# Kernel optimization log

Measured on AMD Instinct MI355X. Metric: run time of the kernel, lower is better.

Reference implementation:

```python
import jax, jax.numpy as jnp
import numpy as np

D_MODEL = 768
N_HEADS = 8
HEAD_DIM = D_MODEL // N_HEADS
LN_EPS = 1e-5

def setup_inputs() -> dict:
    key = jax.random.key(0)
    k1, k2, k3 = jax.random.split(key, 3)
    B, L = 8, 4096
    x = jax.random.normal(k1, (B, L, D_MODEL), dtype=jnp.float32)
    gamma = jnp.ones((D_MODEL,), dtype=jnp.float32)
    beta = jnp.zeros((D_MODEL,), dtype=jnp.float32)
    # torch Linear weights transposed so forward is x @ W
    w_qkv = jax.random.normal(k2, (D_MODEL, 3 * D_MODEL), dtype=jnp.float32) * (1.0 / np.sqrt(D_MODEL))
    w_out = jax.random.normal(k3, (D_MODEL, D_MODEL), dtype=jnp.float32) * (1.0 / np.sqrt(D_MODEL))
    return {"x": x, "gamma": gamma, "beta": beta, "w_qkv": w_qkv, "w_out": w_out}

def reference(x, gamma, beta, w_qkv, w_out):
    B, L, D = x.shape
    residual = x
    # LayerNorm
    mu = jnp.mean(x, axis=-1, keepdims=True)
    var = jnp.mean(jnp.square(x - mu), axis=-1, keepdims=True)
    xn = (x - mu) * jax.lax.rsqrt(var + LN_EPS) * gamma + beta
    # qkv projection, split, reshape to [B, H, L, d]
    qkv = xn @ w_qkv  # [B, L, 3D]
    q, k, v = jnp.split(qkv, 3, axis=-1)
    def to_heads(t):
        return t.reshape(B, L, N_HEADS, HEAD_DIM).transpose(0, 2, 1, 3)
    q, k, v = to_heads(q), to_heads(k), to_heads(v)
    # feature maps: elu + 1
    q = jax.nn.elu(q) + 1.0
    k = jax.nn.elu(k) + 1.0
    # linear attention: kv aggregation then query readout
    kv = jnp.einsum('bhld,bhlv->bhdv', k, v)          # [B,H,d,d]
    out = jnp.einsum('bhld,bhdv->bhlv', q, kv)         # [B,H,L,d]
    k_sum = jnp.sum(k, axis=2)                         # [B,H,d]
    normalizer = jnp.einsum('bhld,bhd->bhl', q, k_sum) # [B,H,L]
    normalizer = jnp.maximum(normalizer, 1e-6)
    out = out / normalizer[..., None]
    out = out.transpose(0, 2, 1, 3).reshape(B, L, D)
    out = out @ w_out
    return out + residual
```

## Files before the change

### kernel.cpp

```cpp
#include <hip/hip_runtime.h>
#include <stdint.h>

#define D_MODEL 768
#define N3      2304
#define NHEAD   8
#define DH      96
#define BATCH   8
#define SEQ     4096
#define ROWS    (BATCH*SEQ)
#define LN_EPS  1e-5f

typedef __attribute__((ext_vector_type(8))) __bf16 bf16x8;
typedef __attribute__((ext_vector_type(4))) float f32x4;
typedef __attribute__((ext_vector_type(8))) unsigned short ushort8;
typedef __attribute__((ext_vector_type(4))) unsigned short ushort4v;

__device__ __forceinline__ unsigned short f2bf(float f) {
  union { float f; unsigned int u; } v; v.f = f;
  unsigned int r = v.u + 0x7FFFu + ((v.u >> 16) & 1u);
  return (unsigned short)(r >> 16);
}
__device__ __forceinline__ float bf2f(unsigned short u) {
  union { unsigned int u; float f; } v; v.u = ((unsigned int)u) << 16;
  return v.f;
}

#define GLOBAL_LDS16(src, dst) \
  __builtin_amdgcn_global_load_lds((const __attribute__((address_space(1))) void*)(src), \
                                   (__attribute__((address_space(3))) void*)(dst), 16, 0, 0)

#define GATE(n) do { asm volatile("s_waitcnt vmcnt(" #n ")" ::: "memory"); \
                     __builtin_amdgcn_s_barrier(); asm volatile("" ::: "memory"); } while (0)

__global__ __launch_bounds__(256) void prep_kernel(
    const float* __restrict__ wqkv, const float* __restrict__ wout,
    unsigned short* __restrict__ wqkvT, unsigned short* __restrict__ woutT,
    const float* __restrict__ x, const float* __restrict__ gamma,
    const float* __restrict__ beta, unsigned short* __restrict__ xn) {
  if (blockIdx.x < 2304) {
    __shared__ float tile[32][33];
    int v = blockIdx.x;
    int bx = v % 96, by = v / 96;
    const float* in; unsigned short* out; int C, c0;
    if (bx < 72) { in = wqkv; out = wqkvT; C = N3;      c0 = bx * 32; }
    else         { in = wout; out = woutT; C = D_MODEL; c0 = (bx - 72) * 32; }
    int r0 = by * 32;
    int tx = threadIdx.x & 31, ty = threadIdx.x >> 5;
    #pragma unroll
    for (int i = ty; i < 32; i += 8)
      tile[i][tx] = in[(size_t)(r0 + i) * C + c0 + tx];
    __syncthreads();
    #pragma unroll
    for (int i = ty; i < 32; i += 8)
      out[(size_t)(c0 + i) * D_MODEL + r0 + tx] = f2bf(tile[tx][i]);
    return;
  }
  int wave = threadIdx.x >> 6, lane = threadIdx.x & 63;
  int row = (blockIdx.x - 2304) * 4 + wave;
  const float* xr = x + (size_t)row * D_MODEL;
  f32x4 v[3];
  float s = 0.f, sq = 0.f;
  #pragma unroll
  for (int i = 0; i < 3; ++i) {
    v[i] = *(const f32x4*)(xr + (i * 64 + lane) * 4);
    #pragma unroll
    for (int c = 0; c < 4; ++c) { s += v[i][c]; sq += v[i][c] * v[i][c]; }
  }
  #pragma unroll
  for (int o = 32; o; o >>= 1) {
    s  += __shfl_xor(s, o, 64);
    sq += __shfl_xor(sq, o, 64);
  }
  float mu  = s * (1.f / 768.f);
  float var = sq * (1.f / 768.f) - mu * mu;
  float rs  = rsqrtf(var + LN_EPS);
  #pragma unroll
  for (int i = 0; i < 3; ++i) {
    int col = (i * 64 + lane) * 4;
    ushort4v o;
    #pragma unroll
    for (int c = 0; c < 4; ++c)
      o[c] = f2bf((v[i][c] - mu) * rs * gamma[col + c] + beta[col + c]);
    *(ushort4v*)(xn + (size_t)row * D_MODEL + col) = o;
  }
}

__global__ __launch_bounds__(256, 2) void gemm_qkv_w_kernel(
    const unsigned short* __restrict__ A, const unsigned short* __restrict__ Bt,
    unsigned short* __restrict__ qb, unsigned short* __restrict__ kT,
    unsigned short* __restrict__ vT) {
  __shared__ unsigned short As[3 * 4096];
  __shared__ unsigned short Bs[3 * 8192];
  const int K = D_MODEL, nbn = 9;
  int nwg = gridDim.x, id = blockIdx.x;
  int q8 = nwg >> 3;
  int wg = (id & 7) * q8 + (id >> 3);
  int bm = wg / nbn, bn = wg % nbn;

  const int lane = threadIdx.x & 63, wid = threadIdx.x >> 6;
  const int wn = wid;
  const int l15 = lane & 15, hi = lane >> 4;
  const int colS = (hi ^ ((l15 >> 1) & 3)) << 3;
  const int srow = lane >> 2;
  const int scol = ((lane & 3) ^ ((lane >> 3) & 3)) << 3;

  const unsigned short* a0 = A  + (size_t)(bm * 128 +      wid * 16 + srow) * K + scol;
  const unsigned short* a1 = A  + (size_t)(bm * 128 + 64 + wid * 16 + srow) * K + scol;
  const unsigned short* b0 = Bt + (size_t)(bn * 256 + wid * 64 +      srow) * K + scol;
  const unsigned short* b1 = Bt + (size_t)(bn * 256 + wid * 64 + 16 + srow) * K + scol;
  const unsigned short* b2 = Bt + (size_t)(bn * 256 + wid * 64 + 32 + srow) * K + scol;
  const unsigned short* b3 = Bt + (size_t)(bn * 256 + wid * 64 + 48 + srow) * K + scol;
  auto stage = [&](int buf, int kt) {
    GLOBAL_LDS16(a0 + kt * 32, &As[buf * 4096 +        wid * 512]);
    GLOBAL_LDS16(a1 + kt * 32, &As[buf * 4096 + 2048 + wid * 512]);
    GLOBAL_LDS16(b0 + kt * 32, &Bs[buf * 8192 + wid * 2048]);
    GLOBAL_LDS16(b1 + kt * 32, &Bs[buf * 8192 + wid * 2048 + 512]);
    GLOBAL_LDS16(b2 + kt * 32, &Bs[buf * 8192 + wid * 2048 + 1024]);
    GLOBAL_LDS16(b3 + kt * 32, &Bs[buf * 8192 + wid * 2048 + 1536]);
  };

  f32x4 acc[8][4];
  #pragma unroll
  for (int i = 0; i < 8; ++i)
    #pragma unroll
    for (int j = 0; j < 4; ++j) acc[i][j] = (f32x4){0.f, 0.f, 0.f, 0.f};

#define QTILE(BUF, STG) do { \
    bf16x8 af[8], bv[4]; \
    _Pragma("unroll") for (int mf = 0; mf < 8; ++mf) \
      af[mf] = *(const bf16x8*)&As[(BUF) * 4096 + (mf * 16 + l15) * 32 + colS]; \
    _Pragma("unroll") for (int nf = 0; nf < 4; ++nf) \
      bv[nf] = *(const bf16x8*)&Bs[(BUF) * 8192 + (wn * 64 + nf * 16 + l15) * 32 + colS]; \
    STG; \
    __builtin_amdgcn_s_setprio(1); \
    _Pragma("unroll") for (int mf = 0; mf < 8; ++mf) \
      _Pragma("unroll") for (int nf = 0; nf < 4; ++nf) \
        acc[mf][nf] = __builtin_amdgcn_mfma_f32_16x16x32_bf16( \
            af[mf], bv[nf], acc[mf][nf], 0, 0, 0); \
    __builtin_amdgcn_s_setprio(0); \
  } while (0)

  stage(0, 0); stage(1, 1);
  for (int it = 0; it < 7; ++it) {
    int T = 3 * it;
    GATE(6); QTILE(0, stage(2, T + 2));
    GATE(6); QTILE(1, stage(0, T + 3));
    GATE(6); QTILE(2, stage(1, T + 4));
  }
  GATE(6); QTILE(0, stage(2, 23));
  GATE(6); QTILE(1, {});
  GATE(0); QTILE(2, {});
#undef QTILE

  int r0 = bm * 128, c0 = bn * 256 + wn * 64;
  if (bn < 3) {
    #pragma unroll
    for (int mf = 0; mf < 8; ++mf)
      #pragma unroll
      for (int nf = 0; nf < 4; ++nf) {
        int col = c0 + nf * 16 + l15;
        #pragma unroll
        for (int r = 0; r < 4; ++r) {
          int row = r0 + mf * 16 + hi * 4 + r;
          float v = acc[mf][nf][r];
          v = (v > 0.f) ? v + 1.f : __expf(v);
          qb[(size_t)row * D_MODEL + col] = f2bf(v);
        }
      }
  } else {
    const bool isK = (bn < 6);
    unsigned short* T = isK ? kT : vT;
    int cbase = c0 - (isK ? 768 : 1536);
    #pragma unroll
    for (int mf = 0; mf < 8; ++mf) {
      int ll = mf * 16 + hi * 4;
      #pragma unroll
      for (int nf = 0; nf < 4; ++nf) {
        int cc = cbase + nf * 16 + l15;
        int h = cc / 96, d = cc - h * 96;
        ushort4v pk;
        #pragma unroll
        for (int r = 0; r < 4; ++r) {
          float v = acc[mf][nf][r];
          if (isK) v = (v > 0.f) ? v + 1.f : __expf(v);
          pk[r] = f2bf(v);
        }
        *(ushort4v*)&T[(((size_t)bm * 8 + h) * 96 + d) * 128 + ll] = pk;
      }
    }
  }
}

__global__ __launch_bounds__(256) void kvagg3_kernel(
    const unsigned short* __restrict__ kT, const unsigned short* __restrict__ vT,
    float* __restrict__ kvp) {
  __shared__ unsigned short KTs[3 * 6144];
  __shared__ unsigned short VTs[3 * 6144];
  __shared__ unsigned short PH[2048];
  int bh = blockIdx.x >> 3, chunk = blockIdx.x & 7;
  int tid = threadIdx.x;
  int lane = tid & 63, wid = tid >> 6;
  int l15 = lane & 15, hi = lane >> 4;

  {
    int r = tid >> 3, sl = tid & 7;
    unsigned short val = (r == 0) ? (unsigned short)0x3F80 : (unsigned short)0;
    ushort8 v8 = {val, val, val, val, val, val, val, val};
    *(ushort8*)&PH[(r * 8 + sl) * 8] = v8;
  }
  __syncthreads();

  const int b = bh >> 3, h = bh & 7;
  auto stage = [&](int buf, int t) {
    #pragma unroll
    for (int i = 0; i < 3; ++i) {
      int sidx = i * 256 + tid;
      int row = sidx >> 3;
      int L = (sidx & 7) ^ (row & 7);
      size_t g = ((((size_t)b * 32 + chunk * 4 + (t >> 1)) * 8 + h) * 96 + row) * 128
               + (t & 1) * 64 + L * 8;
      GLOBAL_LDS16(kT + g, &KTs[buf * 6144 + (i * 256 + wid * 64) * 8]);
      GLOBAL_LDS16(vT + g, &VTs[buf * 6144 + (i * 256 + wid * 64) * 8]);
    }
  };

  f32x4 acc[6][2];
  #pragma unroll
  for (int i = 0; i < 6; ++i)
    #pragma unroll
    for (int j = 0; j < 2; ++j) acc[i][j] = (f32x4){0.f, 0.f, 0.f, 0.f};

#define KVTILE(BUF) do { \
    _Pragma("unroll") for (int kq = 0; kq < 2; ++kq) { \
      bf16x8 af[6], bv[2]; \
      _Pragma("unroll") for (int mf = 0; mf < 6; ++mf) { \
        int row = mf * 16 + l15; \
        af[mf] = *(const bf16x8*)&KTs[(BUF) * 6144 + row * 64 + ((kq * 4 + hi) ^ (row & 7)) * 8]; } \
      if (wid < 3) { \
        _Pragma("unroll") for (int nf = 0; nf < 2; ++nf) { \
          int row = wid * 32 + nf * 16 + l15; \
          bv[nf] = *(const bf16x8*)&VTs[(BUF) * 6144 + row * 64 + ((kq * 4 + hi) ^ (row & 7)) * 8]; } \
      } else { \
        _Pragma("unroll") for (int nf = 0; nf < 2; ++nf) { \
          int row = nf * 16 + l15; \
          bv[nf] = *(const bf16x8*)&PH[row * 64 + ((kq * 4 + hi) ^ ((row + 96) & 7)) * 8]; } \
      } \
      __builtin_amdgcn_s_setprio(1); \
      _Pragma("unroll") for (int mf = 0; mf < 6; ++mf) \
        _Pragma("unroll") for (int nf = 0; nf < 2; ++nf) \
          acc[mf][nf] = __builtin_amdgcn_mfma_f32_16x16x32_bf16( \
              af[mf], bv[nf], acc[mf][nf], 0, 0, 0); \
      __builtin_amdgcn_s_setprio(0); \
    } } while (0)

  stage(0, 0); stage(1, 1);
  for (int t = 0; t < 6; ++t) {
    stage((t + 2) % 3, t + 2);
    GATE(12);
    KVTILE(t % 3);
  }
  GATE(6); KVTILE(0);
  GATE(0); KVTILE(1);
#undef KVTILE

  float* outp = kvp + ((size_t)bh * 8 + chunk) * (96 * 112);
  #pragma unroll
  for (int nf = 0; nf < 2; ++nf) {
    int e = wid * 32 + nf * 16 + l15;
    if (e < 112) {
      #pragma unroll
      for (int mf = 0; mf < 6; ++mf)
        #pragma unroll
        for (int r = 0; r < 4; ++r) {
          int d = mf * 16 + hi * 4 + r;
          outp[d * 112 + e] = acc[mf][nf][r];
        }
    }
  }
}

__global__ __launch_bounds__(256) void kvreduce2_kernel(
    const float* __restrict__ kvp, unsigned short* __restrict__ kvN,
    float* __restrict__ ksumf) {
  int idx = blockIdx.x * 256 + threadIdx.x;
  if (idx >= 64 * 96 * 112) return;
  int e = idx % 112;
  int d = (idx / 112) % 96;
  int bh = idx / (112 * 96);
  float s = 0.f;
  #pragma unroll
  for (int c = 0; c < 8; ++c)
    s += kvp[(((size_t)bh * 8 + c) * 96 + d) * 112 + e];
  if (e < 96)       kvN[((size_t)bh * 96 + d) * 96 + e] = f2bf(s);
  else if (e == 96) ksumf[(size_t)bh * 96 + d] = s;
}

__global__ __launch_bounds__(256) void mid_kernel(
    const unsigned short* __restrict__ kvN, const unsigned short* __restrict__ woutT,
    unsigned short* __restrict__ Mt,
    const unsigned short* __restrict__ qb, const float* __restrict__ ksumf,
    unsigned short* __restrict__ qhat) {
  if (blockIdx.x < 192) {
    int bx = blockIdx.x;
    int cb = bx % 3, h = (bx / 3) % 8, b = bx / 24;
    int bh = b * 8 + h;
    const int lane = threadIdx.x & 63, wid = threadIdx.x >> 6;
    const int l15 = lane & 15, hi = lane >> 4;

    f32x4 acc[6][4];
    #pragma unroll
    for (int i = 0; i < 6; ++i)
      #pragma unroll
      for (int j = 0; j < 4; ++j) acc[i][j] = (f32x4){0.f, 0.f, 0.f, 0.f};

    #pragma unroll
    for (int kq = 0; kq < 3; ++kq) {
      int e = kq * 32 + hi * 8;
      bf16x8 af[6], bv[4];
      #pragma unroll
      for (int rf = 0; rf < 6; ++rf) {
        int d = rf * 16 + l15;
        af[rf] = *(const bf16x8*)&kvN[((size_t)bh * 96 + d) * 96 + e];
      }
      #pragma unroll
      for (int cf = 0; cf < 4; ++cf) {
        int c = cb * 256 + wid * 64 + cf * 16 + l15;
        bv[cf] = *(const bf16x8*)&woutT[(size_t)c * 768 + h * 96 + e];
      }
      #pragma unroll
      for (int rf = 0; rf < 6; ++rf)
        #pragma unroll
        for (int cf = 0; cf < 4; ++cf)
          acc[rf][cf] = __builtin_amdgcn_mfma_f32_16x16x32_bf16(
              af[rf], bv[cf], acc[rf][cf], 0, 0, 0);
    }

    #pragma unroll
    for (int rf = 0; rf < 6; ++rf) {
      int hd = h * 96 + rf * 16 + hi * 4;
      #pragma unroll
      for (int cf = 0; cf < 4; ++cf) {
        int c = cb * 256 + wid * 64 + cf * 16 + l15;
        ushort4v pk;
        #pragma unroll
        for (int r = 0; r < 4; ++r) pk[r] = f2bf(acc[rf][cf][r]);
        *(ushort4v*)&Mt[(size_t)b * 589824 + (size_t)c * 768 + hd] = pk;
      }
    }
    return;
  }
  __shared__ float ks[8][96];
  int tid = threadIdx.x;
  int row0 = (blockIdx.x - 192) * 64;
  int b = row0 >> 12;
  #pragma unroll
  for (int i = 0; i < 3; ++i) {
    int idx = i * 256 + tid;
    if (idx < 768) ks[idx / 96][idx % 96] = ksumf[(size_t)b * 768 + idx];
  }
  __syncthreads();

  int row = row0 + (tid >> 2), seg = tid & 3;
  size_t base = (size_t)row * D_MODEL + seg * 192;
  ushort8 qreg[24];
  #pragma unroll
  for (int c = 0; c < 24; ++c)
    qreg[c] = *(const ushort8*)(qb + base + c * 8);

  float inv[2];
  #pragma unroll
  for (int hh = 0; hh < 2; ++hh) {
    int h = seg * 2 + hh;
    float n = 0.f;
    #pragma unroll
    for (int c = 0; c < 12; ++c)
      #pragma unroll
      for (int j = 0; j < 8; ++j)
        n += bf2f(qreg[hh * 12 + c][j]) * ks[h][c * 8 + j];
    inv[hh] = 1.f / fmaxf(n, 1e-6f);
  }
  #pragma unroll
  for (int c = 0; c < 24; ++c) {
    float sc = inv[c / 12];
    ushort8 o;
    #pragma unroll
    for (int j = 0; j < 8; ++j) o[j] = f2bf(bf2f(qreg[c][j]) * sc);
    *(ushort8*)(qhat + base + c * 8) = o;
  }
}

__global__ __launch_bounds__(256, 2) void gemm_fin_kernel(
    const unsigned short* __restrict__ A, const unsigned short* __restrict__ MtAll,
    const float* __restrict__ resid, float* __restrict__ Cf) {
  __shared__ unsigned short As[3 * 4096];
  __shared__ unsigned short Bs[3 * 8192];
  const int K = D_MODEL, nbn = 3;
  int nwg = gridDim.x, id = blockIdx.x;
  int q8 = nwg >> 3;
  int wg = (id & 7) * q8 + (id >> 3);
  int bm = wg / nbn, bn = wg % nbn;
  const unsigned short* Bt = MtAll + (size_t)(bm >> 5) * 589824;

  const int lane = threadIdx.x & 63, wid = threadIdx.x >> 6;
  const int wn = wid;
  const int l15 = lane & 15, hi = lane >> 4;
  const int colS = (hi ^ ((l15 >> 1) & 3)) << 3;
  const int srow = lane >> 2;
  const int scol = ((lane & 3) ^ ((lane >> 3) & 3)) << 3;

  const unsigned short* a0 = A  + (size_t)(bm * 128 +      wid * 16 + srow) * K + scol;
  const unsigned short* a1 = A  + (size_t)(bm * 128 + 64 + wid * 16 + srow) * K + scol;
  const unsigned short* b0 = Bt + (size_t)(bn * 256 + wid * 64 +      srow) * K + scol;
  const unsigned short* b1 = Bt + (size_t)(bn * 256 + wid * 64 + 16 + srow) * K + scol;
  const unsigned short* b2 = Bt + (size_t)(bn * 256 + wid * 64 + 32 + srow) * K + scol;
  const unsigned short* b3 = Bt + (size_t)(bn * 256 + wid * 64 + 48 + srow) * K + scol;
  auto stage = [&](int buf, int kt) {
    GLOBAL_LDS16(a0 + kt * 32, &As[buf * 4096 +        wid * 512]);
    GLOBAL_LDS16(a1 + kt * 32, &As[buf * 4096 + 2048 + wid * 512]);
    GLOBAL_LDS16(b0 + kt * 32, &Bs[buf * 8192 + wid * 2048]);
    GLOBAL_LDS16(b1 + kt * 32, &Bs[buf * 8192 + wid * 2048 + 512]);
    GLOBAL_LDS16(b2 + kt * 32, &Bs[buf * 8192 + wid * 2048 + 1024]);
    GLOBAL_LDS16(b3 + kt * 32, &Bs[buf * 8192 + wid * 2048 + 1536]);
  };

  f32x4 acc[8][4];
  #pragma unroll
  for (int i = 0; i < 8; ++i)
    #pragma unroll
    for (int j = 0; j < 4; ++j) acc[i][j] = (f32x4){0.f, 0.f, 0.f, 0.f};

#define FTILE(BUF, STG) do { \
    bf16x8 af[8], bv[4]; \
    _Pragma("unroll") for (int mf = 0; mf < 8; ++mf) \
      af[mf] = *(const bf16x8*)&As[(BUF) * 4096 + (mf * 16 + l15) * 32 + colS]; \
    _Pragma("unroll") for (int nf = 0; nf < 4; ++nf) \
      bv[nf] = *(const bf16x8*)&Bs[(BUF) * 8192 + (wn * 64 + nf * 16 + l15) * 32 + colS]; \
    STG; \
    __builtin_amdgcn_s_setprio(1); \
    _Pragma("unroll") for (int mf = 0; mf < 8; ++mf) \
      _Pragma("unroll") for (int nf = 0; nf < 4; ++nf) \
        acc[mf][nf] = __builtin_amdgcn_mfma_f32_16x16x32_bf16( \
            af[mf], bv[nf], acc[mf][nf], 0, 0, 0); \
    __builtin_amdgcn_s_setprio(0); \
  } while (0)

  stage(0, 0); stage(1, 1);
  for (int it = 0; it < 7; ++it) {
    int T = 3 * it;
    GATE(6); FTILE(0, stage(2, T + 2));
    GATE(6); FTILE(1, stage(0, T + 3));
    GATE(6); FTILE(2, stage(1, T + 4));
  }
  GATE(6); FTILE(0, stage(2, 23));
  GATE(6); FTILE(1, {});
  GATE(0); FTILE(2, {});
#undef FTILE

  int r0 = bm * 128, c0 = bn * 256 + wn * 64;
  #pragma unroll
  for (int mf = 0; mf < 8; ++mf)
    #pragma unroll
    for (int nf = 0; nf < 4; ++nf) {
      int col = c0 + nf * 16 + l15;
      #pragma unroll
      for (int r = 0; r < 4; ++r) {
        int row = r0 + mf * 16 + hi * 4 + r;
        Cf[(size_t)row * D_MODEL + col] =
            acc[mf][nf][r] + resid[(size_t)row * D_MODEL + col];
      }
    }
}

extern "C" void kernel_launch(void* const* d_in, const int* in_sizes, int n_in,
                              void* d_out, int out_size, void* d_ws, size_t ws_size,
                              hipStream_t stream) {
  const float* x     = (const float*)d_in[0];
  const float* gamma = (const float*)d_in[1];
  const float* beta  = (const float*)d_in[2];
  const float* w_qkv = (const float*)d_in[3];
  const float* w_out = (const float*)d_in[4];
  float* out = (float*)d_out;

  char* ws = (char*)d_ws;
  size_t off = 0;
  auto alloc = [&](size_t bytes) -> void* {
    void* p = ws + off; off += (bytes + 255) & ~(size_t)255; return p;
  };
  unsigned short* xn    = (unsigned short*)alloc((size_t)ROWS * D_MODEL * 2);
  unsigned short* qb    = (unsigned short*)alloc((size_t)ROWS * D_MODEL * 2);
  unsigned short* kTb   = (unsigned short*)alloc((size_t)64 * 96 * SEQ * 2);
  unsigned short* vTb   = (unsigned short*)alloc((size_t)64 * 96 * SEQ * 2);
  unsigned short* wqkvT = (unsigned short*)alloc((size_t)N3 * D_MODEL * 2);
  unsigned short* woutT = (unsigned short*)alloc((size_t)D_MODEL * D_MODEL * 2);
  float* kvp            = (float*)alloc((size_t)512 * 96 * 112 * 4);
  unsigned short* kvN   = (unsigned short*)alloc((size_t)64 * 96 * 96 * 2);
  float* ksumf          = (float*)alloc((size_t)64 * 96 * 4);
  unsigned short* Mt    = (unsigned short*)alloc((size_t)BATCH * 768 * 768 * 2);

  prep_kernel<<<2304 + ROWS / 4, 256, 0, stream>>>(w_qkv, w_out, wqkvT, woutT,
                                                   x, gamma, beta, xn);
  gemm_qkv_w_kernel<<<(ROWS / 128) * (N3 / 256), 256, 0, stream>>>(xn, wqkvT, qb, kTb, vTb);
  kvagg3_kernel<<<512, 256, 0, stream>>>(kTb, vTb, kvp);
  kvreduce2_kernel<<<(64 * 96 * 112 + 255) / 256, 256, 0, stream>>>(kvp, kvN, ksumf);
  mid_kernel<<<192 + ROWS / 64, 256, 0, stream>>>(kvN, woutT, Mt, qb, ksumf, xn);
  gemm_fin_kernel<<<(ROWS / 128) * 3, 256, 0, stream>>>(xn, Mt, x, out);
}
```

Measured before the change: 312.2 us.

## Fuse kv chunk reduction into mid kernel and shrink GEMM N-tiles to 192

Removes the separate kvreduce2 kernel: mid2 now sums the eight fp32 kv partial chunks directly when loading its MFMA operands and when building the k-sum, which saves a launch and a round trip through a bf16 intermediate. Both large GEMMs also move from 128x256 to 128x192 tiles (three N fragments per wave, smaller LDS B buffers), which gives more workgroups and possibly better occupancy or tail balance. In exchange, the partial sums are recomputed redundantly in mid2 blocks (the k-sum once per qhat block), and the smaller tiles have lower arithmetic intensity per tile.

```diff
diff --git a/kernel.cpp b/kernel.cpp
--- a/kernel.cpp
+++ b/kernel.cpp
@@ -90,15 +90,14 @@
     unsigned short* __restrict__ qb, unsigned short* __restrict__ kT,
     unsigned short* __restrict__ vT) {
   __shared__ unsigned short As[3 * 4096];
-  __shared__ unsigned short Bs[3 * 8192];
-  const int K = D_MODEL, nbn = 9;
+  __shared__ unsigned short Bs[3 * 6144];
+  const int K = D_MODEL, nbn = 12;
   int nwg = gridDim.x, id = blockIdx.x;
   int q8 = nwg >> 3;
   int wg = (id & 7) * q8 + (id >> 3);
   int bm = wg / nbn, bn = wg % nbn;
 
   const int lane = threadIdx.x & 63, wid = threadIdx.x >> 6;
-  const int wn = wid;
   const int l15 = lane & 15, hi = lane >> 4;
   const int colS = (hi ^ ((l15 >> 1) & 3)) << 3;
   const int srow = lane >> 2;
@@ -106,35 +105,33 @@
 
   const unsigned short* a0 = A  + (size_t)(bm * 128 +      wid * 16 + srow) * K + scol;
   const unsigned short* a1 = A  + (size_t)(bm * 128 + 64 + wid * 16 + srow) * K + scol;
-  const unsigned short* b0 = Bt + (size_t)(bn * 256 + wid * 64 +      srow) * K + scol;
-  const unsigned short* b1 = Bt + (size_t)(bn * 256 + wid * 64 + 16 + srow) * K + scol;
-  const unsigned short* b2 = Bt + (size_t)(bn * 256 + wid * 64 + 32 + srow) * K + scol;
-  const unsigned short* b3 = Bt + (size_t)(bn * 256 + wid * 64 + 48 + srow) * K + scol;
+  const unsigned short* b0 = Bt + (size_t)(bn * 192 + wid * 48 +      srow) * K + scol;
+  const unsigned short* b1 = Bt + (size_t)(bn * 192 + wid * 48 + 16 + srow) * K + scol;
+  const unsigned short* b2 = Bt + (size_t)(bn * 192 + wid * 48 + 32 + srow) * K + scol;
   auto stage = [&](int buf, int kt) {
     GLOBAL_LDS16(a0 + kt * 32, &As[buf * 4096 +        wid * 512]);
     GLOBAL_LDS16(a1 + kt * 32, &As[buf * 4096 + 2048 + wid * 512]);
-    GLOBAL_LDS16(b0 + kt * 32, &Bs[buf * 8192 + wid * 2048]);
-    GLOBAL_LDS16(b1 + kt * 32, &Bs[buf * 8192 + wid * 2048 + 512]);
-    GLOBAL_LDS16(b2 + kt * 32, &Bs[buf * 8192 + wid * 2048 + 1024]);
-    GLOBAL_LDS16(b3 + kt * 32, &Bs[buf * 8192 + wid * 2048 + 1536]);
+    GLOBAL_LDS16(b0 + kt * 32, &Bs[buf * 6144 + wid * 1536]);
+    GLOBAL_LDS16(b1 + kt * 32, &Bs[buf * 6144 + wid * 1536 + 512]);
+    GLOBAL_LDS16(b2 + kt * 32, &Bs[buf * 6144 + wid * 1536 + 1024]);
   };
 
-  f32x4 acc[8][4];
+  f32x4 acc[8][3];
   #pragma unroll
   for (int i = 0; i < 8; ++i)
     #pragma unroll
-    for (int j = 0; j < 4; ++j) acc[i][j] = (f32x4){0.f, 0.f, 0.f, 0.f};
+    for (int j = 0; j < 3; ++j) acc[i][j] = (f32x4){0.f, 0.f, 0.f, 0.f};
 
 #define QTILE(BUF, STG) do { \
-    bf16x8 af[8], bv[4]; \
+    bf16x8 af[8], bv[3]; \
     _Pragma("unroll") for (int mf = 0; mf < 8; ++mf) \
       af[mf] = *(const bf16x8*)&As[(BUF) * 4096 + (mf * 16 + l15) * 32 + colS]; \
-    _Pragma("unroll") for (int nf = 0; nf < 4; ++nf) \
-      bv[nf] = *(const bf16x8*)&Bs[(BUF) * 8192 + (wn * 64 + nf * 16 + l15) * 32 + colS]; \
+    _Pragma("unroll") for (int nf = 0; nf < 3; ++nf) \
+      bv[nf] = *(const bf16x8*)&Bs[(BUF) * 6144 + (wid * 48 + nf * 16 + l15) * 32 + colS]; \
     STG; \
     __builtin_amdgcn_s_setprio(1); \
     _Pragma("unroll") for (int mf = 0; mf < 8; ++mf) \
-      _Pragma("unroll") for (int nf = 0; nf < 4; ++nf) \
+      _Pragma("unroll") for (int nf = 0; nf < 3; ++nf) \
         acc[mf][nf] = __builtin_amdgcn_mfma_f32_16x16x32_bf16( \
             af[mf], bv[nf], acc[mf][nf], 0, 0, 0); \
     __builtin_amdgcn_s_setprio(0); \
@@ -143,21 +140,21 @@
   stage(0, 0); stage(1, 1);
   for (int it = 0; it < 7; ++it) {
     int T = 3 * it;
-    GATE(6); QTILE(0, stage(2, T + 2));
-    GATE(6); QTILE(1, stage(0, T + 3));
-    GATE(6); QTILE(2, stage(1, T + 4));
-  }
-  GATE(6); QTILE(0, stage(2, 23));
-  GATE(6); QTILE(1, {});
+    GATE(5); QTILE(0, stage(2, T + 2));
+    GATE(5); QTILE(1, stage(0, T + 3));
+    GATE(5); QTILE(2, stage(1, T + 4));
+  }
+  GATE(5); QTILE(0, stage(2, 23));
+  GATE(5); QTILE(1, {});
   GATE(0); QTILE(2, {});
 #undef QTILE
 
-  int r0 = bm * 128, c0 = bn * 256 + wn * 64;
-  if (bn < 3) {
+  int r0 = bm * 128, c0 = bn * 192 + wid * 48;
+  if (bn < 4) {
     #pragma unroll
     for (int mf = 0; mf < 8; ++mf)
       #pragma unroll
-      for (int nf = 0; nf < 4; ++nf) {
+      for (int nf = 0; nf < 3; ++nf) {
         int col = c0 + nf * 16 + l15;
         #pragma unroll
         for (int r = 0; r < 4; ++r) {
@@ -168,14 +165,14 @@
         }
       }
   } else {
-    const bool isK = (bn < 6);
+    const bool isK = (bn < 8);
     unsigned short* T = isK ? kT : vT;
     int cbase = c0 - (isK ? 768 : 1536);
     #pragma unroll
     for (int mf = 0; mf < 8; ++mf) {
       int ll = mf * 16 + hi * 4;
       #pragma unroll
-      for (int nf = 0; nf < 4; ++nf) {
+      for (int nf = 0; nf < 3; ++nf) {
         int cc = cbase + nf * 16 + l15;
         int h = cc / 96, d = cc - h * 96;
         ushort4v pk;
@@ -279,33 +276,17 @@
   }
 }
 
-__global__ __launch_bounds__(256) void kvreduce2_kernel(
-    const float* __restrict__ kvp, unsigned short* __restrict__ kvN,
-    float* __restrict__ ksumf) {
-  int idx = blockIdx.x * 256 + threadIdx.x;
-  if (idx >= 64 * 96 * 112) return;
-  int e = idx % 112;
-  int d = (idx / 112) % 96;
-  int bh = idx / (112 * 96);
-  float s = 0.f;
-  #pragma unroll
-  for (int c = 0; c < 8; ++c)
-    s += kvp[(((size_t)bh * 8 + c) * 96 + d) * 112 + e];
-  if (e < 96)       kvN[((size_t)bh * 96 + d) * 96 + e] = f2bf(s);
-  else if (e == 96) ksumf[(size_t)bh * 96 + d] = s;
-}
-
-__global__ __launch_bounds__(256) void mid_kernel(
-    const unsigned short* __restrict__ kvN, const unsigned short* __restrict__ woutT,
+__global__ __launch_bounds__(256) void mid2_kernel(
+    const float* __restrict__ kvp, const unsigned short* __restrict__ woutT,
     unsigned short* __restrict__ Mt,
-    const unsigned short* __restrict__ qb, const float* __restrict__ ksumf,
-    unsigned short* __restrict__ qhat) {
+    const unsigned short* __restrict__ qb, unsigned short* __restrict__ qhat) {
   if (blockIdx.x < 192) {
     int bx = blockIdx.x;
     int cb = bx % 3, h = (bx / 3) % 8, b = bx / 24;
     int bh = b * 8 + h;
     const int lane = threadIdx.x & 63, wid = threadIdx.x >> 6;
     const int l15 = lane & 15, hi = lane >> 4;
+    const float* kp = kvp + (size_t)bh * 8 * 96 * 112;
 
     f32x4 acc[6][4];
     #pragma unroll
@@ -315,17 +296,27 @@
 
     #pragma unroll
     for (int kq = 0; kq < 3; ++kq) {
-      int e = kq * 32 + hi * 8;
+      int e0 = kq * 32 + hi * 8;
       bf16x8 af[6], bv[4];
       #pragma unroll
       for (int rf = 0; rf < 6; ++rf) {
         int d = rf * 16 + l15;
-        af[rf] = *(const bf16x8*)&kvN[((size_t)bh * 96 + d) * 96 + e];
+        f32x4 sa = {0.f, 0.f, 0.f, 0.f}, sb = {0.f, 0.f, 0.f, 0.f};
+        #pragma unroll
+        for (int c = 0; c < 8; ++c) {
+          const float* p = kp + ((size_t)c * 96 + d) * 112 + e0;
+          sa += *(const f32x4*)p;
+          sb += *(const f32x4*)(p + 4);
+        }
+        ushort8 tmp;
+        #pragma unroll
+        for (int j = 0; j < 4; ++j) { tmp[j] = f2bf(sa[j]); tmp[4 + j] = f2bf(sb[j]); }
+        af[rf] = *(const bf16x8*)&tmp;
       }
       #pragma unroll
       for (int cf = 0; cf < 4; ++cf) {
         int c = cb * 256 + wid * 64 + cf * 16 + l15;
-        bv[cf] = *(const bf16x8*)&woutT[(size_t)c * 768 + h * 96 + e];
+        bv[cf] = *(const bf16x8*)&woutT[(size_t)c * 768 + h * 96 + e0];
       }
       #pragma unroll
       for (int rf = 0; rf < 6; ++rf)
@@ -356,7 +347,14 @@
   #pragma unroll
   for (int i = 0; i < 3; ++i) {
     int idx = i * 256 + tid;
-    if (idx < 768) ks[idx / 96][idx % 96] = ksumf[(size_t)b * 768 + idx];
+    if (idx < 768) {
+      int h = idx / 96, d = idx % 96;
+      const float* p = kvp + (((size_t)(b * 8 + h) * 8) * 96 + d) * 112 + 96;
+      float s = 0.f;
+      #pragma unroll
+      for (int c = 0; c < 8; ++c) s += p[(size_t)c * 96 * 112];
+      ks[h][d] = s;
+    }
   }
   __syncthreads();
 
@@ -393,8 +391,8 @@
     const unsigned short* __restrict__ A, const unsigned short* __restrict__ MtAll,
     const float* __restrict__ resid, float* __restrict__ Cf) {
   __shared__ unsigned short As[3 * 4096];
-  __shared__ unsigned short Bs[3 * 8192];
-  const int K = D_MODEL, nbn = 3;
+  __shared__ unsigned short Bs[3 * 6144];
+  const int K = D_MODEL, nbn = 4;
   int nwg = gridDim.x, id = blockIdx.x;
   int q8 = nwg >> 3;
   int wg = (id & 7) * q8 + (id >> 3);
@@ -402,7 +400,6 @@
   const unsigned short* Bt = MtAll + (size_t)(bm >> 5) * 589824;
 
   const int lane = threadIdx.x & 63, wid = threadIdx.x >> 6;
-  const int wn = wid;
   const int l15 = lane & 15, hi = lane >> 4;
   const int colS = (hi ^ ((l15 >> 1) & 3)) << 3;
   const int srow = lane >> 2;
@@ -410,35 +407,33 @@
 
   const unsigned short* a0 = A  + (size_t)(bm * 128 +      wid * 16 + srow) * K + scol;
   const unsigned short* a1 = A  + (size_t)(bm * 128 + 64 + wid * 16 + srow) * K + scol;
-  const unsigned short* b0 = Bt + (size_t)(bn * 256 + wid * 64 +      srow) * K + scol;
-  const unsigned short* b1 = Bt + (size_t)(bn * 256 + wid * 64 + 16 + srow) * K + scol;
-  const unsigned short* b2 = Bt + (size_t)(bn * 256 + wid * 64 + 32 + srow) * K + scol;
-  const unsigned short* b3 = Bt + (size_t)(bn * 256 + wid * 64 + 48 + srow) * K + scol;
+  const unsigned short* b0 = Bt + (size_t)(bn * 192 + wid * 48 +      srow) * K + scol;
+  const unsigned short* b1 = Bt + (size_t)(bn * 192 + wid * 48 + 16 + srow) * K + scol;
+  const unsigned short* b2 = Bt + (size_t)(bn * 192 + wid * 48 + 32 + srow) * K + scol;
   auto stage = [&](int buf, int kt) {
     GLOBAL_LDS16(a0 + kt * 32, &As[buf * 4096 +        wid * 512]);
     GLOBAL_LDS16(a1 + kt * 32, &As[buf * 4096 + 2048 + wid * 512]);
-    GLOBAL_LDS16(b0 + kt * 32, &Bs[buf * 8192 + wid * 2048]);
-    GLOBAL_LDS16(b1 + kt * 32, &Bs[buf * 8192 + wid * 2048 + 512]);
-    GLOBAL_LDS16(b2 + kt * 32, &Bs[buf * 8192 + wid * 2048 + 1024]);
-    GLOBAL_LDS16(b3 + kt * 32, &Bs[buf * 8192 + wid * 2048 + 1536]);
+    GLOBAL_LDS16(b0 + kt * 32, &Bs[buf * 6144 + wid * 1536]);
+    GLOBAL_LDS16(b1 + kt * 32, &Bs[buf * 6144 + wid * 1536 + 512]);
+    GLOBAL_LDS16(b2 + kt * 32, &Bs[buf * 6144 + wid * 1536 + 1024]);
   };
 
-  f32x4 acc[8][4];
+  f32x4 acc[8][3];
   #pragma unroll
   for (int i = 0; i < 8; ++i)
     #pragma unroll
-    for (int j = 0; j < 4; ++j) acc[i][j] = (f32x4){0.f, 0.f, 0.f, 0.f};
+    for (int j = 0; j < 3; ++j) acc[i][j] = (f32x4){0.f, 0.f, 0.f, 0.f};
 
 #define FTILE(BUF, STG) do { \
-    bf16x8 af[8], bv[4]; \
+    bf16x8 af[8], bv[3]; \
     _Pragma("unroll") for (int mf = 0; mf < 8; ++mf) \
       af[mf] = *(const bf16x8*)&As[(BUF) * 4096 + (mf * 16 + l15) * 32 + colS]; \
-    _Pragma("unroll") for (int nf = 0; nf < 4; ++nf) \
-      bv[nf] = *(const bf16x8*)&Bs[(BUF) * 8192 + (wn * 64 + nf * 16 + l15) * 32 + colS]; \
+    _Pragma("unroll") for (int nf = 0; nf < 3; ++nf) \
+      bv[nf] = *(const bf16x8*)&Bs[(BUF) * 6144 + (wid * 48 + nf * 16 + l15) * 32 + colS]; \
     STG; \
     __builtin_amdgcn_s_setprio(1); \
     _Pragma("unroll") for (int mf = 0; mf < 8; ++mf) \
-      _Pragma("unroll") for (int nf = 0; nf < 4; ++nf) \
+      _Pragma("unroll") for (int nf = 0; nf < 3; ++nf) \
         acc[mf][nf] = __builtin_amdgcn_mfma_f32_16x16x32_bf16( \
             af[mf], bv[nf], acc[mf][nf], 0, 0, 0); \
     __builtin_amdgcn_s_setprio(0); \
@@ -447,20 +442,20 @@
   stage(0, 0); stage(1, 1);
   for (int it = 0; it < 7; ++it) {
     int T = 3 * it;
-    GATE(6); FTILE(0, stage(2, T + 2));
-    GATE(6); FTILE(1, stage(0, T + 3));
-    GATE(6); FTILE(2, stage(1, T + 4));
-  }
-  GATE(6); FTILE(0, stage(2, 23));
-  GATE(6); FTILE(1, {});
+    GATE(5); FTILE(0, stage(2, T + 2));
+    GATE(5); FTILE(1, stage(0, T + 3));
+    GATE(5); FTILE(2, stage(1, T + 4));
+  }
+  GATE(5); FTILE(0, stage(2, 23));
+  GATE(5); FTILE(1, {});
   GATE(0); FTILE(2, {});
 #undef FTILE
 
-  int r0 = bm * 128, c0 = bn * 256 + wn * 64;
+  int r0 = bm * 128, c0 = bn * 192 + wid * 48;
   #pragma unroll
   for (int mf = 0; mf < 8; ++mf)
     #pragma unroll
-    for (int nf = 0; nf < 4; ++nf) {
+    for (int nf = 0; nf < 3; ++nf) {
       int col = c0 + nf * 16 + l15;
       #pragma unroll
       for (int r = 0; r < 4; ++r) {
@@ -493,15 +488,12 @@
   unsigned short* wqkvT = (unsigned short*)alloc((size_t)N3 * D_MODEL * 2);
   unsigned short* woutT = (unsigned short*)alloc((size_t)D_MODEL * D_MODEL * 2);
   float* kvp            = (float*)alloc((size_t)512 * 96 * 112 * 4);
-  unsigned short* kvN   = (unsigned short*)alloc((size_t)64 * 96 * 96 * 2);
-  float* ksumf          = (float*)alloc((size_t)64 * 96 * 4);
   unsigned short* Mt    = (unsigned short*)alloc((size_t)BATCH * 768 * 768 * 2);
 
   prep_kernel<<<2304 + ROWS / 4, 256, 0, stream>>>(w_qkv, w_out, wqkvT, woutT,
                                                    x, gamma, beta, xn);
-  gemm_qkv_w_kernel<<<(ROWS / 128) * (N3 / 256), 256, 0, stream>>>(xn, wqkvT, qb, kTb, vTb);
+  gemm_qkv_w_kernel<<<(ROWS / 128) * (N3 / 192), 256, 0, stream>>>(xn, wqkvT, qb, kTb, vTb);
   kvagg3_kernel<<<512, 256, 0, stream>>>(kTb, vTb, kvp);
-  kvreduce2_kernel<<<(64 * 96 * 112 + 255) / 256, 256, 0, stream>>>(kvp, kvN, ksumf);
-  mid_kernel<<<192 + ROWS / 64, 256, 0, stream>>>(kvN, woutT, Mt, qb, ksumf, xn);
-  gemm_fin_kernel<<<(ROWS / 128) * 3, 256, 0, stream>>>(xn, Mt, x, out);
-}
+  mid2_kernel<<<192 + ROWS / 64, 256, 0, stream>>>(kvp, woutT, Mt, qb, xn);
+  gemm_fin_kernel<<<(ROWS / 128) * 4, 256, 0, stream>>>(xn, Mt, x, out);
+}
```

Result: slower. 337.1 us (+8.0%).
